# Optimization experiments

Measured on AMD Instinct MI355X. Metric: run time of the kernel, lower is better.

Reference implementation:

```python
import jax, jax.numpy as jnp
import numpy as np

D_MODEL = 1024
HEADS = 16


def setup_inputs() -> dict:
    key = jax.random.key(0)
    ks = jax.random.split(key, 11)
    B, S, D = 2, 2048, D_MODEL
    scale = 1.0 / np.sqrt(D)
    inp = {
        "q": jax.random.normal(ks[0], (B, S, D), jnp.float32),
        "k": jax.random.normal(ks[1], (B, S, D), jnp.float32),
        "v": jax.random.normal(ks[2], (B, S, D), jnp.float32),
        "w_q": jax.random.normal(ks[3], (D, D), jnp.float32) * scale,
        "b_q": jnp.zeros((D,), jnp.float32),
        "w_k": jax.random.normal(ks[4], (D, D), jnp.float32) * scale,
        "b_k": jnp.zeros((D,), jnp.float32),
        "w_v": jax.random.normal(ks[5], (D, D), jnp.float32) * scale,
        "b_v": jnp.zeros((D,), jnp.float32),
        "w_o": jax.random.normal(ks[6], (D, D), jnp.float32) * scale,
        "b_o": jnp.zeros((D,), jnp.float32),
    }
    return inp


def reference(q, k, v, w_q, b_q, w_k, b_k, w_v, b_v, w_o, b_o):
    B, S, D = q.shape
    H = HEADS
    Dh = D // H

    def split(x):  # [B,S,D] -> [B,H,S,Dh]
        return x.reshape(B, S, H, Dh).transpose(0, 2, 1, 3)

    qh = split(q @ w_q + b_q)
    kh = split(k @ w_k + b_k)
    vh = split(v @ w_v + b_v)

    # scaled dot-product attention: softmax(Q K^T / sqrt(Dh)) V
    scores = jnp.einsum("bhsd,bhtd->bhst", qh, kh) / jnp.sqrt(
        jnp.asarray(Dh, qh.dtype)
    )
    attn = jax.nn.softmax(scores, axis=-1)
    out = jnp.einsum("bhst,bhtd->bhsd", attn, vh)

    concat = out.transpose(0, 2, 1, 3).reshape(B, S, D)
    return concat @ w_o + b_o
```

## Files before the change

### kernel.cpp

```cpp
#include <hip/hip_runtime.h>
#include <hip/hip_bf16.h>
#include <math.h>

using bf16 = __hip_bfloat16;
typedef __bf16 bf16x8v __attribute__((ext_vector_type(8)));
typedef float f32x4v __attribute__((ext_vector_type(4)));

#define AS1 __attribute__((address_space(1)))
#define AS3 __attribute__((address_space(3)))

__device__ __forceinline__ void g2l16(const void* g, void* l) {
  __builtin_amdgcn_global_load_lds((const AS1 void*)g, (AS3 void*)l, 16, 0, 0);
}

__device__ __forceinline__ float fclamp(float v) {
  return fminf(fmaxf(v, -6.0e4f), 6.0e4f);
}

__device__ __forceinline__ unsigned packbf(float a, float b) {
  unsigned short lo = __builtin_bit_cast(unsigned short, __float2bfloat16(a));
  unsigned short hi = __builtin_bit_cast(unsigned short, __float2bfloat16(b));
  return (unsigned)lo | ((unsigned)hi << 16);
}

#define QSCL 0.1803368801111204f

__global__ __launch_bounds__(256) void transpose_cvt4(
    const float* __restrict__ w0, const float* __restrict__ w1,
    const float* __restrict__ w2, const float* __restrict__ w3,
    bf16* __restrict__ o0, bf16* __restrict__ o1,
    bf16* __restrict__ o2, bf16* __restrict__ o3) {
  const float* in = (blockIdx.z == 0) ? w0 : (blockIdx.z == 1) ? w1
                    : (blockIdx.z == 2) ? w2 : w3;
  bf16* out = (blockIdx.z == 0) ? o0 : (blockIdx.z == 1) ? o1
              : (blockIdx.z == 2) ? o2 : o3;
  __shared__ alignas(16) bf16 tile[64][80];
  const int t = threadIdx.x;
  const int bx = blockIdx.x * 64, by = blockIdx.y * 64;
#pragma unroll
  for (int p = 0; p < 4; ++p) {
    int idx = p * 1024 + t * 4;
    int r = idx >> 6, c0 = idx & 63;
    float4 v = *(const float4*)&in[(size_t)(by + r) * 1024 + bx + c0];
    tile[c0 + 0][r] = __float2bfloat16(v.x);
    tile[c0 + 1][r] = __float2bfloat16(v.y);
    tile[c0 + 2][r] = __float2bfloat16(v.z);
    tile[c0 + 3][r] = __float2bfloat16(v.w);
  }
  __syncthreads();
#pragma unroll
  for (int p = 0; p < 2; ++p) {
    int idx = p * 2048 + t * 8;
    int c = idx >> 6, r0 = idx & 63;
    *(uint4*)&out[(size_t)(bx + c) * 1024 + by + r0] = *(const uint4*)&tile[c][r0];
  }
}

__global__ __launch_bounds__(256) void cvt3(
    const float* __restrict__ q, const float* __restrict__ k,
    const float* __restrict__ v, bf16* __restrict__ oq,
    bf16* __restrict__ ok, bf16* __restrict__ ov) {
  const float* in = (blockIdx.y == 0) ? q : (blockIdx.y == 1) ? k : v;
  bf16* out = (blockIdx.y == 0) ? oq : (blockIdx.y == 1) ? ok : ov;
  int i = (blockIdx.x * 256 + threadIdx.x) * 8;
  float4 a = *(const float4*)&in[i];
  float4 b = *(const float4*)&in[i + 4];
  alignas(16) bf16 tmp[8];
  tmp[0] = __float2bfloat16(a.x); tmp[1] = __float2bfloat16(a.y);
  tmp[2] = __float2bfloat16(a.z); tmp[3] = __float2bfloat16(a.w);
  tmp[4] = __float2bfloat16(b.x); tmp[5] = __float2bfloat16(b.y);
  tmp[6] = __float2bfloat16(b.z); tmp[7] = __float2bfloat16(b.w);
  *(uint4*)&out[i] = *(const uint4*)tmp;
}

__device__ __forceinline__ void qkv_store(bf16* C, int z, int m, int n, float v) {
  int b_ = m >> 11, s_ = m & 2047, h_ = n >> 6, d_ = n & 63;
  size_t oidx = (z == 2)
      ? ((size_t)(b_ * 16 + h_) * 64 + d_) * 2048 + s_
      : ((size_t)(b_ * 16 + h_) * 2048 + s_) * 64 + d_;
  C[oidx] = __float2bfloat16(v);
}

__global__ __launch_bounds__(256, 2) void gemm_qkv_bf16(
    const bf16* __restrict__ Aq, const bf16* __restrict__ Ak,
    const bf16* __restrict__ Av,
    const bf16* __restrict__ WtQ, const bf16* __restrict__ WtK,
    const bf16* __restrict__ WtV,
    const float* __restrict__ bq, const float* __restrict__ bk_,
    const float* __restrict__ bv_,
    bf16* __restrict__ Qh, bf16* __restrict__ Kh, bf16* __restrict__ Vt) {
  constexpr int K = 1024;
  const int z = blockIdx.z;
  const bf16* A    = (z == 0) ? Aq : (z == 1) ? Ak : Av;
  const bf16* Bt   = (z == 0) ? WtQ : (z == 1) ? WtK : WtV;
  const float* bias = (z == 0) ? bq : (z == 1) ? bk_ : bv_;
  bf16* C = (z == 0) ? Qh : (z == 1) ? Kh : Vt;

  __shared__ alignas(16) bf16 As[128 * 32];
  __shared__ alignas(16) bf16 Bs[128 * 32];
  const int t = threadIdx.x;
  const int wave = t >> 6, lane = t & 63;
  const int quad = lane >> 4, l16 = lane & 15;
  const int bm = blockIdx.x * 128, bn = blockIdx.y * 128;
  const int wm = (wave & 1) * 64, wn = (wave >> 1) * 64;

  f32x4v acc[4][4] = {};

  for (int k0 = 0; k0 < K; k0 += 32) {
    __syncthreads();
#pragma unroll
    for (int c = 0; c < 2; ++c) {
      int idx = c * 2048 + t * 8;
      int row = idx >> 5, col = idx & 31;
      g2l16(&A[(size_t)(bm + row) * K + k0 + col], &As[c * 2048 + wave * 512]);
      g2l16(&Bt[(size_t)(bn + row) * K + k0 + col], &Bs[c * 2048 + wave * 512]);
    }
    __syncthreads();

    bf16x8v a[4], b[4];
#pragma unroll
    for (int mi = 0; mi < 4; ++mi)
      a[mi] = *(const bf16x8v*)&As[(wm + mi * 16 + l16) * 32 + quad * 8];
#pragma unroll
    for (int ni = 0; ni < 4; ++ni)
      b[ni] = *(const bf16x8v*)&Bs[(wn + ni * 16 + l16) * 32 + quad * 8];
#pragma unroll
    for (int mi = 0; mi < 4; ++mi)
#pragma unroll
      for (int ni = 0; ni < 4; ++ni)
        acc[mi][ni] = __builtin_amdgcn_mfma_f32_16x16x32_bf16(a[mi], b[ni],
                                                              acc[mi][ni], 0, 0, 0);
  }

  if (z == 2) {
#pragma unroll
    for (int ni = 0; ni < 4; ++ni) {
      int n = bn + wn + ni * 16 + l16;
      float bz = bias[n];
      int h_ = n >> 6, d_ = n & 63;
#pragma unroll
      for (int mi = 0; mi < 4; ++mi) {
        int m0 = bm + wm + mi * 16 + quad * 4;
        int b_ = m0 >> 11, s0 = m0 & 2047;
        uint2 u;
        u.x = packbf(fclamp(acc[mi][ni][0] + bz), fclamp(acc[mi][ni][1] + bz));
        u.y = packbf(fclamp(acc[mi][ni][2] + bz), fclamp(acc[mi][ni][3] + bz));
        *(uint2*)&C[((size_t)(b_ * 16 + h_) * 64 + d_) * 2048 + s0] = u;
      }
    }
  } else {
    const float scl = (z == 0) ? QSCL : 1.0f;
#pragma unroll
    for (int ni = 0; ni < 4; ++ni) {
      int n = bn + wn + ni * 16 + l16;
      float bz = bias[n];
#pragma unroll
      for (int mi = 0; mi < 4; ++mi)
#pragma unroll
        for (int r = 0; r < 4; ++r) {
          int m = bm + wm + mi * 16 + quad * 4 + r;
          qkv_store(C, z, m, n, fclamp(acc[mi][ni][r] + bz) * scl);
        }
    }
  }
}

__global__ __launch_bounds__(256, 2) void gemm_qkv_f32(
    const float* __restrict__ Aq, const float* __restrict__ Ak,
    const float* __restrict__ Av,
    const bf16* __restrict__ WtQ, const bf16* __restrict__ WtK,
    const bf16* __restrict__ WtV,
    const float* __restrict__ bq, const float* __restrict__ bk_,
    const float* __restrict__ bv_,
    bf16* __restrict__ Qh, bf16* __restrict__ Kh, bf16* __restrict__ Vt) {
  constexpr int K = 1024, LDA = 40;
  const int z = blockIdx.z;
  const float* A  = (z == 0) ? Aq : (z == 1) ? Ak : Av;
  const bf16* Bt  = (z == 0) ? WtQ : (z == 1) ? WtK : WtV;
  const float* bias = (z == 0) ? bq : (z == 1) ? bk_ : bv_;
  bf16* C = (z == 0) ? Qh : (z == 1) ? Kh : Vt;

  __shared__ alignas(16) bf16 As[128 * LDA];
  __shared__ alignas(16) bf16 Bs[128 * LDA];
  const int t = threadIdx.x;
  const int wave = t >> 6, lane = t & 63;
  const int quad = lane >> 4, l16 = lane & 15;
  const int bm = blockIdx.x * 128, bn = blockIdx.y * 128;
  const int wm = (wave & 1) * 64, wn = (wave >> 1) * 64;

  f32x4v acc[4][4] = {};

  for (int k0 = 0; k0 < K; k0 += 32) {
    uint4 va[2], vb[2];
#pragma unroll
    for (int c = 0; c < 2; ++c) {
      int idx = c * 2048 + t * 8;
      int row = idx >> 5, col = idx & 31;
      const float* src = &A[(size_t)(bm + row) * K + k0 + col];
      float4 f0 = *(const float4*)src;
      float4 f1 = *(const float4*)(src + 4);
      alignas(16) bf16 tmp[8];
      tmp[0] = __float2bfloat16(f0.x); tmp[1] = __float2bfloat16(f0.y);
      tmp[2] = __float2bfloat16(f0.z); tmp[3] = __float2bfloat16(f0.w);
      tmp[4] = __float2bfloat16(f1.x); tmp[5] = __float2bfloat16(f1.y);
      tmp[6] = __float2bfloat16(f1.z); tmp[7] = __float2bfloat16(f1.w);
      va[c] = *(const uint4*)tmp;
      vb[c] = *(const uint4*)&Bt[(size_t)(bn + row) * K + k0 + col];
    }
    __syncthreads();
#pragma unroll
    for (int c = 0; c < 2; ++c) {
      int idx = c * 2048 + t * 8;
      int row = idx >> 5, col = idx & 31;
      *(uint4*)&As[row * LDA + col] = va[c];
      *(uint4*)&Bs[row * LDA + col] = vb[c];
    }
    __syncthreads();

    bf16x8v a[4], b[4];
#pragma unroll
    for (int mi = 0; mi < 4; ++mi)
      a[mi] = *(const bf16x8v*)&As[(wm + mi * 16 + l16) * LDA + quad * 8];
#pragma unroll
    for (int ni = 0; ni < 4; ++ni)
      b[ni] = *(const bf16x8v*)&Bs[(wn + ni * 16 + l16) * LDA + quad * 8];
#pragma unroll
    for (int mi = 0; mi < 4; ++mi)
#pragma unroll
      for (int ni = 0; ni < 4; ++ni)
        acc[mi][ni] = __builtin_amdgcn_mfma_f32_16x16x32_bf16(a[mi], b[ni],
                                                              acc[mi][ni], 0, 0, 0);
  }

  if (z == 2) {
#pragma unroll
    for (int ni = 0; ni < 4; ++ni) {
      int n = bn + wn + ni * 16 + l16;
      float bz = bias[n];
      int h_ = n >> 6, d_ = n & 63;
#pragma unroll
      for (int mi = 0; mi < 4; ++mi) {
        int m0 = bm + wm + mi * 16 + quad * 4;
        int b_ = m0 >> 11, s0 = m0 & 2047;
        uint2 u;
        u.x = packbf(fclamp(acc[mi][ni][0] + bz), fclamp(acc[mi][ni][1] + bz));
        u.y = packbf(fclamp(acc[mi][ni][2] + bz), fclamp(acc[mi][ni][3] + bz));
        *(uint2*)&C[((size_t)(b_ * 16 + h_) * 64 + d_) * 2048 + s0] = u;
      }
    }
  } else {
    const float scl = (z == 0) ? QSCL : 1.0f;
#pragma unroll
    for (int ni = 0; ni < 4; ++ni) {
      int n = bn + wn + ni * 16 + l16;
      float bz = bias[n];
#pragma unroll
      for (int mi = 0; mi < 4; ++mi)
#pragma unroll
        for (int r = 0; r < 4; ++r) {
          int m = bm + wm + mi * 16 + quad * 4 + r;
          qkv_store(C, z, m, n, fclamp(acc[mi][ni][r] + bz) * scl);
        }
    }
  }
}

__global__ __launch_bounds__(256, 2) void gemm_out(
    const bf16* __restrict__ A, const bf16* __restrict__ Bt,
    const float* __restrict__ bias, float* __restrict__ C) {
  constexpr int K = 1024, N = 1024;
  __shared__ alignas(16) bf16 As[128 * 32];
  __shared__ alignas(16) bf16 Bs[64 * 32];
  const int t = threadIdx.x;
  const int wave = t >> 6, lane = t & 63;
  const int quad = lane >> 4, l16 = lane & 15;
  const int bm = blockIdx.x * 128, bn = blockIdx.y * 64;
  const int wm = (wave & 1) * 64, wn = (wave >> 1) * 32;

  f32x4v acc[4][2] = {};

  for (int k0 = 0; k0 < K; k0 += 32) {
    __syncthreads();
#pragma unroll
    for (int c = 0; c < 2; ++c) {
      int idx = c * 2048 + t * 8;
      int row = idx >> 5, col = idx & 31;
      g2l16(&A[(size_t)(bm + row) * K + k0 + col], &As[c * 2048 + wave * 512]);
    }
    {
      int idx = t * 8;
      int row = idx >> 5, col = idx & 31;
      g2l16(&Bt[(size_t)(bn + row) * K + k0 + col], &Bs[wave * 512]);
    }
    __syncthreads();

    bf16x8v a[4], b[2];
#pragma unroll
    for (int mi = 0; mi < 4; ++mi)
      a[mi] = *(const bf16x8v*)&As[(wm + mi * 16 + l16) * 32 + quad * 8];
#pragma unroll
    for (int ni = 0; ni < 2; ++ni)
      b[ni] = *(const bf16x8v*)&Bs[(wn + ni * 16 + l16) * 32 + quad * 8];
#pragma unroll
    for (int mi = 0; mi < 4; ++mi)
#pragma unroll
      for (int ni = 0; ni < 2; ++ni)
        acc[mi][ni] = __builtin_amdgcn_mfma_f32_16x16x32_bf16(a[mi], b[ni],
                                                              acc[mi][ni], 0, 0, 0);
  }

#pragma unroll
  for (int ni = 0; ni < 2; ++ni) {
    int n = bn + wn + ni * 16 + l16;
    float bz = bias[n];
#pragma unroll
    for (int mi = 0; mi < 4; ++mi)
#pragma unroll
      for (int r = 0; r < 4; ++r) {
        int m = bm + wm + mi * 16 + quad * 4 + r;
        C[(size_t)m * N + n] = fclamp(acc[mi][ni][r] + bz);
      }
  }
}

__global__ __launch_bounds__(256, 2) void attn(
    const bf16* __restrict__ Qh, const bf16* __restrict__ Kh,
    const bf16* __restrict__ Vt, bf16* __restrict__ Ctx) {
  constexpr int LDPP = 40;
  __shared__ alignas(16) bf16 QsPs[128 * 64];
  __shared__ alignas(16) bf16 Ks[3][64 * 64];
  __shared__ alignas(16) bf16 Vs[3][64 * 64];
  const int t = threadIdx.x;
  const int wave = t >> 6, lane = t & 63;
  const int quad = lane >> 4, l16 = lane & 15;
  const int sw = l16 & 7;

  const int lin = blockIdx.x;
  const int li = lin >> 3;
  const int qb = li & 15;
  const int bh = (lin & 7) * 4 + (li >> 4);

  const size_t bh_off = (size_t)bh * 2048 * 64;
  const bf16* Qb = Qh + bh_off;
  const bf16* Kb = Kh + bh_off;
  const bf16* Vb = Vt + bh_off;

  const int srow = t >> 3;
  const int schunk = t & 7;

  auto stageKV = [&](int kt, int buf) {
#pragma unroll
    for (int c = 0; c < 2; ++c) {
      int row = c * 32 + srow;
      int mc = schunk ^ (row & 7);
      g2l16(&Kb[(size_t)(kt * 64 + row) * 64 + mc * 8],
            &Ks[buf][c * 2048 + wave * 512]);
      g2l16(&Vb[(size_t)row * 2048 + kt * 64 + mc * 8],
            &Vs[buf][c * 2048 + wave * 512]);
    }
  };

#pragma unroll
  for (int c = 0; c < 4; ++c) {
    int row = c * 32 + srow;
    int mc = schunk ^ (row & 7);
    g2l16(&Qb[(size_t)(qb * 128 + row) * 64 + mc * 8],
          &QsPs[c * 2048 + wave * 512]);
  }
  stageKV(0, 0);
  asm volatile("s_waitcnt vmcnt(4)" ::: "memory");
  __builtin_amdgcn_s_barrier();

  bf16x8v aq[2][2];
#pragma unroll
  for (int mi = 0; mi < 2; ++mi)
#pragma unroll
    for (int kk = 0; kk < 2; ++kk)
      aq[mi][kk] = *(const bf16x8v*)
          &QsPs[(wave * 32 + mi * 16 + l16) * 64 + (((kk * 4 + quad) ^ sw) << 3)];

  __syncthreads();
  bf16* Psw = QsPs + wave * (32 * LDPP);

  stageKV(1, 1);

  bf16x8v vone;
#pragma unroll
  for (int i = 0; i < 8; ++i) vone[i] = (__bf16)1.0f;

  f32x4v lsum[2] = {};
  f32x4v oacc[2][4] = {};

  auto compute = [&](int buf) {
#pragma unroll
    for (int h = 0; h < 2; ++h) {
      f32x4v s[2][2] = {};
      __builtin_amdgcn_s_setprio(1);
#pragma unroll
      for (int kk = 0; kk < 2; ++kk)
#pragma unroll
        for (int ni = 0; ni < 2; ++ni) {
          bf16x8v bk = *(const bf16x8v*)
              &Ks[buf][(h * 32 + ni * 16 + l16) * 64 + (((kk * 4 + quad) ^ sw) << 3)];
#pragma unroll
          for (int mi = 0; mi < 2; ++mi)
            s[mi][ni] = __builtin_amdgcn_mfma_f32_16x16x32_bf16(bk, aq[mi][kk],
                                                                s[mi][ni], 0, 0, 0);
        }
      __builtin_amdgcn_s_setprio(0);

#pragma unroll
      for (int mi = 0; mi < 2; ++mi)
#pragma unroll
        for (int ni = 0; ni < 2; ++ni) {
          float p0 = __builtin_amdgcn_exp2f(fminf(s[mi][ni][0], 80.f));
          float p1 = __builtin_amdgcn_exp2f(fminf(s[mi][ni][1], 80.f));
          float p2 = __builtin_amdgcn_exp2f(fminf(s[mi][ni][2], 80.f));
          float p3 = __builtin_amdgcn_exp2f(fminf(s[mi][ni][3], 80.f));
          uint2 u;
          u.x = packbf(p0, p1);
          u.y = packbf(p2, p3);
          *(uint2*)&Psw[(mi * 16 + l16) * LDPP + ni * 16 + quad * 4] = u;
        }

      bf16x8v ap[2];
#pragma unroll
      for (int mi = 0; mi < 2; ++mi)
        ap[mi] = *(const bf16x8v*)&Psw[(mi * 16 + l16) * LDPP + quad * 8];
      __builtin_amdgcn_s_setprio(1);
#pragma unroll
      for (int mi = 0; mi < 2; ++mi)
        lsum[mi] = __builtin_amdgcn_mfma_f32_16x16x32_bf16(ap[mi], vone,
                                                           lsum[mi], 0, 0, 0);
#pragma unroll
      for (int ni = 0; ni < 4; ++ni) {
        bf16x8v bv = *(const bf16x8v*)
            &Vs[buf][(ni * 16 + l16) * 64 + (((h * 4 + quad) ^ sw) << 3)];
#pragma unroll
        for (int mi = 0; mi < 2; ++mi)
          oacc[mi][ni] = __builtin_amdgcn_mfma_f32_16x16x32_bf16(ap[mi], bv,
                                                                 oacc[mi][ni],
                                                                 0, 0, 0);
      }
      __builtin_amdgcn_s_setprio(0);
    }
  };

  int bufc = 0;
  for (int tt = 0; tt < 30; ++tt) {
    int bufs = bufc + 2; if (bufs >= 3) bufs -= 3;
    stageKV(tt + 2, bufs);
    compute(bufc);
    asm volatile("s_waitcnt vmcnt(4)" ::: "memory");
    __builtin_amdgcn_s_barrier();
    bufc = (bufc == 2) ? 0 : bufc + 1;
  }
  compute(bufc);
  asm volatile("s_waitcnt vmcnt(0)" ::: "memory");
  __builtin_amdgcn_s_barrier();
  bufc = (bufc == 2) ? 0 : bufc + 1;
  compute(bufc);

  const int b_ = bh >> 4, h_ = bh & 15;
#pragma unroll
  for (int mi = 0; mi < 2; ++mi)
#pragma unroll
    for (int r = 0; r < 4; ++r) {
      int sr = qb * 128 + wave * 32 + mi * 16 + quad * 4 + r;
      float inv = 1.0f / fmaxf(lsum[mi][r], 1.0e-20f);
#pragma unroll
      for (int ni = 0; ni < 4; ++ni) {
        int col = h_ * 64 + ni * 16 + l16;
        Ctx[(size_t)(b_ * 2048 + sr) * 1024 + col] =
            __float2bfloat16(fclamp(oacc[mi][ni][r] * inv));
      }
    }
}

extern "C" void kernel_launch(void* const* d_in, const int* in_sizes, int n_in,
                              void* d_out, int out_size, void* d_ws, size_t ws_size,
                              hipStream_t stream) {
  const float* q   = (const float*)d_in[0];
  const float* k   = (const float*)d_in[1];
  const float* v   = (const float*)d_in[2];
  const float* w_q = (const float*)d_in[3];
  const float* b_q = (const float*)d_in[4];
  const float* w_k = (const float*)d_in[5];
  const float* b_k = (const float*)d_in[6];
  const float* w_v = (const float*)d_in[7];
  const float* b_v = (const float*)d_in[8];
  const float* w_o = (const float*)d_in[9];
  const float* b_o = (const float*)d_in[10];
  float* out = (float*)d_out;

  char* ws = (char*)d_ws;
  const size_t MB = (size_t)1024 * 1024;
  bf16* WtQ = (bf16*)(ws + 0 * MB);
  bf16* WtK = (bf16*)(ws + 2 * MB);
  bf16* WtV = (bf16*)(ws + 4 * MB);
  bf16* WtO = (bf16*)(ws + 6 * MB);

  dim3 tb(256);
  transpose_cvt4<<<dim3(16, 16, 4), tb, 0, stream>>>(w_q, w_k, w_v, w_o,
                                                     WtQ, WtK, WtV, WtO);

  const bool big = ws_size >= (size_t)57 * MB;
  if (big) {
    bf16* Qa  = (bf16*)(ws + 8 * MB);
    bf16* Ka  = (bf16*)(ws + 16 * MB);
    bf16* Va  = (bf16*)(ws + 24 * MB);
    bf16* Qh  = (bf16*)(ws + 32 * MB);
    bf16* Kh  = (bf16*)(ws + 40 * MB);
    bf16* Vt  = (bf16*)(ws + 48 * MB);
    bf16* Ctx = Qa;

    cvt3<<<dim3(2048, 3), tb, 0, stream>>>(q, k, v, Qa, Ka, Va);
    gemm_qkv_bf16<<<dim3(32, 8, 3), tb, 0, stream>>>(Qa, Ka, Va, WtQ, WtK, WtV,
                                                     b_q, b_k, b_v, Qh, Kh, Vt);
    attn<<<dim3(512), tb, 0, stream>>>(Qh, Kh, Vt, Ctx);
    gemm_out<<<dim3(32, 16), tb, 0, stream>>>(Ctx, WtO, b_o, out);
  } else {
    bf16* Qh  = (bf16*)(ws + 8 * MB);
    bf16* Kh  = (bf16*)(ws + 16 * MB);
    bf16* Vt  = (bf16*)(ws + 24 * MB);
    bf16* Ctx = (bf16*)(ws + 32 * MB);

    gemm_qkv_f32<<<dim3(32, 8, 3), tb, 0, stream>>>(q, k, v, WtQ, WtK, WtV,
                                                    b_q, b_k, b_v, Qh, Kh, Vt);
    attn<<<dim3(512), tb, 0, stream>>>(Qh, Kh, Vt, Ctx);
    gemm_out<<<dim3(32, 16), tb, 0, stream>>>(Ctx, WtO, b_o, out);
  }
}
```

Measured before the change: 224.7 us.

## Switch attention to 32x32x16 MFMA and pass P through permlane32 swap instead of LDS

Rewrites the attention inner loop to use 32x32x16 bf16 MFMA tiles instead of 16x16x32. For S=QK^T each wave now computes a 32x32 block per instruction, and the output accumulator becomes two 32x32 tiles. The exponentiated probabilities are packed to bf16 and rearranged in registers with v_permlane32_swap so they can be fed directly as the A operand of the PV MFMA. This removes the per-tile LDS round-trip (write P, then read it back) along with the padded P scratch area. The cost is larger per-lane accumulators and therefore more register pressure, plus a dependency on an exact lane layout for the permlane swap.

Result: no change. 228.2 us (+1.5%).

```diff
diff --git a/kernel.cpp b/kernel.cpp
--- a/kernel.cpp
+++ b/kernel.cpp
@@ -5,6 +5,7 @@
 using bf16 = __hip_bfloat16;
 typedef __bf16 bf16x8v __attribute__((ext_vector_type(8)));
 typedef float f32x4v __attribute__((ext_vector_type(4)));
+typedef float f32x16v __attribute__((ext_vector_type(16)));
 
 #define AS1 __attribute__((address_space(1)))
 #define AS3 __attribute__((address_space(3)))
@@ -326,14 +327,13 @@
 __global__ __launch_bounds__(256, 2) void attn(
     const bf16* __restrict__ Qh, const bf16* __restrict__ Kh,
     const bf16* __restrict__ Vt, bf16* __restrict__ Ctx) {
-  constexpr int LDPP = 40;
-  __shared__ alignas(16) bf16 QsPs[128 * 64];
+  __shared__ alignas(16) bf16 Qs[128 * 64];
   __shared__ alignas(16) bf16 Ks[3][64 * 64];
   __shared__ alignas(16) bf16 Vs[3][64 * 64];
   const int t = threadIdx.x;
   const int wave = t >> 6, lane = t & 63;
-  const int quad = lane >> 4, l16 = lane & 15;
-  const int sw = l16 & 7;
+  const int l31 = lane & 31, hi5 = lane >> 5;
+  const int swk = l31 & 7;
 
   const int lin = blockIdx.x;
   const int li = lin >> 3;
@@ -365,22 +365,19 @@
     int row = c * 32 + srow;
     int mc = schunk ^ (row & 7);
     g2l16(&Qb[(size_t)(qb * 128 + row) * 64 + mc * 8],
-          &QsPs[c * 2048 + wave * 512]);
+          &Qs[c * 2048 + wave * 512]);
   }
   stageKV(0, 0);
   asm volatile("s_waitcnt vmcnt(4)" ::: "memory");
   __builtin_amdgcn_s_barrier();
 
-  bf16x8v aq[2][2];
-#pragma unroll
-  for (int mi = 0; mi < 2; ++mi)
-#pragma unroll
-    for (int kk = 0; kk < 2; ++kk)
-      aq[mi][kk] = *(const bf16x8v*)
-          &QsPs[(wave * 32 + mi * 16 + l16) * 64 + (((kk * 4 + quad) ^ sw) << 3)];
+  bf16x8v aq[4];
+#pragma unroll
+  for (int ks = 0; ks < 4; ++ks)
+    aq[ks] = *(const bf16x8v*)
+        &Qs[(wave * 32 + l31) * 64 + (((2 * ks + hi5) ^ swk) << 3)];
 
   __syncthreads();
-  bf16* Psw = QsPs + wave * (32 * LDPP);
 
   stageKV(1, 1);
 
@@ -388,61 +385,53 @@
 #pragma unroll
   for (int i = 0; i < 8; ++i) vone[i] = (__bf16)1.0f;
 
-  f32x4v lsum[2] = {};
-  f32x4v oacc[2][4] = {};
+  f32x16v lacc = {};
+  f32x16v oacc[2] = {};
 
   auto compute = [&](int buf) {
 #pragma unroll
-    for (int h = 0; h < 2; ++h) {
-      f32x4v s[2][2] = {};
+    for (int kg = 0; kg < 2; ++kg) {
+      f32x16v s = {};
       __builtin_amdgcn_s_setprio(1);
 #pragma unroll
-      for (int kk = 0; kk < 2; ++kk)
-#pragma unroll
-        for (int ni = 0; ni < 2; ++ni) {
-          bf16x8v bk = *(const bf16x8v*)
-              &Ks[buf][(h * 32 + ni * 16 + l16) * 64 + (((kk * 4 + quad) ^ sw) << 3)];
-#pragma unroll
-          for (int mi = 0; mi < 2; ++mi)
-            s[mi][ni] = __builtin_amdgcn_mfma_f32_16x16x32_bf16(bk, aq[mi][kk],
-                                                                s[mi][ni], 0, 0, 0);
-        }
-      __builtin_amdgcn_s_setprio(0);
-
-#pragma unroll
-      for (int mi = 0; mi < 2; ++mi)
-#pragma unroll
-        for (int ni = 0; ni < 2; ++ni) {
-          float p0 = __builtin_amdgcn_exp2f(fminf(s[mi][ni][0], 80.f));
-          float p1 = __builtin_amdgcn_exp2f(fminf(s[mi][ni][1], 80.f));
-          float p2 = __builtin_amdgcn_exp2f(fminf(s[mi][ni][2], 80.f));
-          float p3 = __builtin_amdgcn_exp2f(fminf(s[mi][ni][3], 80.f));
-          uint2 u;
-          u.x = packbf(p0, p1);
-          u.y = packbf(p2, p3);
-          *(uint2*)&Psw[(mi * 16 + l16) * LDPP + ni * 16 + quad * 4] = u;
-        }
-
-      bf16x8v ap[2];
-#pragma unroll
-      for (int mi = 0; mi < 2; ++mi)
-        ap[mi] = *(const bf16x8v*)&Psw[(mi * 16 + l16) * LDPP + quad * 8];
-      __builtin_amdgcn_s_setprio(1);
-#pragma unroll
-      for (int mi = 0; mi < 2; ++mi)
-        lsum[mi] = __builtin_amdgcn_mfma_f32_16x16x32_bf16(ap[mi], vone,
-                                                           lsum[mi], 0, 0, 0);
-#pragma unroll
-      for (int ni = 0; ni < 4; ++ni) {
-        bf16x8v bv = *(const bf16x8v*)
-            &Vs[buf][(ni * 16 + l16) * 64 + (((h * 4 + quad) ^ sw) << 3)];
-#pragma unroll
-        for (int mi = 0; mi < 2; ++mi)
-          oacc[mi][ni] = __builtin_amdgcn_mfma_f32_16x16x32_bf16(ap[mi], bv,
-                                                                 oacc[mi][ni],
-                                                                 0, 0, 0);
+      for (int ks = 0; ks < 4; ++ks) {
+        bf16x8v ak = *(const bf16x8v*)
+            &Ks[buf][(kg * 32 + l31) * 64 + (((2 * ks + hi5) ^ swk) << 3)];
+        s = __builtin_amdgcn_mfma_f32_32x32x16_bf16(ak, aq[ks], s, 0, 0, 0);
       }
       __builtin_amdgcn_s_setprio(0);
+
+      float p[16];
+#pragma unroll
+      for (int r = 0; r < 16; ++r)
+        p[r] = __builtin_amdgcn_exp2f(fminf(s[r], 80.f));
+
+#pragma unroll
+      for (int ksl = 0; ksl < 2; ++ksl) {
+        const int rb = ksl * 8;
+        unsigned fa = packbf(p[rb + 0], p[rb + 1]);
+        unsigned fb = packbf(p[rb + 2], p[rb + 3]);
+        unsigned fc = packbf(p[rb + 4], p[rb + 5]);
+        unsigned fd = packbf(p[rb + 6], p[rb + 7]);
+        asm volatile("v_permlane32_swap_b32 %0, %1" : "+v"(fa), "+v"(fc));
+        asm volatile("v_permlane32_swap_b32 %0, %1" : "+v"(fb), "+v"(fd));
+        union { unsigned u[4]; bf16x8v v; } fr;
+        fr.u[0] = fa; fr.u[1] = fb; fr.u[2] = fc; fr.u[3] = fd;
+
+        const int ks = kg * 2 + ksl;
+        __builtin_amdgcn_s_setprio(1);
+        lacc = __builtin_amdgcn_mfma_f32_32x32x16_bf16(fr.v, vone, lacc,
+                                                       0, 0, 0);
+#pragma unroll
+        for (int dblk = 0; dblk < 2; ++dblk) {
+          bf16x8v bv = *(const bf16x8v*)
+              &Vs[buf][(dblk * 32 + l31) * 64 + (((2 * ks + hi5) ^ swk) << 3)];
+          oacc[dblk] = __builtin_amdgcn_mfma_f32_32x32x16_bf16(fr.v, bv,
+                                                               oacc[dblk],
+                                                               0, 0, 0);
+        }
+        __builtin_amdgcn_s_setprio(0);
+      }
     }
   };
 
@@ -463,18 +452,17 @@
 
   const int b_ = bh >> 4, h_ = bh & 15;
 #pragma unroll
-  for (int mi = 0; mi < 2; ++mi)
-#pragma unroll
-    for (int r = 0; r < 4; ++r) {
-      int sr = qb * 128 + wave * 32 + mi * 16 + quad * 4 + r;
-      float inv = 1.0f / fmaxf(lsum[mi][r], 1.0e-20f);
-#pragma unroll
-      for (int ni = 0; ni < 4; ++ni) {
-        int col = h_ * 64 + ni * 16 + l16;
-        Ctx[(size_t)(b_ * 2048 + sr) * 1024 + col] =
-            __float2bfloat16(fclamp(oacc[mi][ni][r] * inv));
-      }
-    }
+  for (int r = 0; r < 16; ++r) {
+    int qrow = (r & 3) + 8 * (r >> 2) + 4 * hi5;
+    int sr = qb * 128 + wave * 32 + qrow;
+    float inv = 1.0f / fmaxf(lacc[r], 1.0e-20f);
+#pragma unroll
+    for (int dblk = 0; dblk < 2; ++dblk) {
+      int col = h_ * 64 + dblk * 32 + l31;
+      Ctx[(size_t)(b_ * 2048 + sr) * 1024 + col] =
+          __float2bfloat16(fclamp(oacc[dblk][r] * inv));
+    }
+  }
 }
 
 extern "C" void kernel_launch(void* const* d_in, const int* in_sizes, int n_in,
```
